# Performance work log

Measured on AMD Instinct MI355X. Metric: run time of the kernel, lower is better.

Reference implementation:

```python
import jax, jax.numpy as jnp
import numpy as np

ANNEAL = 0.01

def _tsig(x, temp=ANNEAL):
    # temperature sigmoid with +/-50 clipping as in the torch source
    return jax.nn.sigmoid(jnp.clip(x / temp, -50.0, 50.0))

def setup_inputs() -> dict:
    key = jax.random.key(0)
    k1, k2 = jax.random.split(key)
    N, D = 512, 512
    preds = jax.random.normal(k1, (N, D), dtype=jnp.float32)
    labels = jax.random.randint(k2, (N,), 0, 64, dtype=jnp.int64)
    return {"preds": preds, "labels": labels}

def reference(preds, labels):
    N = preds.shape[0]
    dtype = preds.dtype
    eye = jnp.eye(N, dtype=dtype)
    same = (labels[:, None] == labels[None, :]).astype(dtype)
    I_pos = same * (1.0 - eye)                      # positives excl. self
    sim_mat = preds @ preds.T                       # [N, N]
    # sim_diff[i, j, k] = sim_mat[i, k] - sim_mat[i, j]
    sim_sg = _tsig(sim_mat[:, None, :] - sim_mat[:, :, None]) * (1.0 - eye)[None, :, :]
    sim_all_rk = 1.0 + jnp.sum(sim_sg, axis=-1)     # [N, N]
    # sum_k sim_sg[i,j,k] * I_pos[i,k]
    pos_sum = jnp.einsum('ijk,ik->ij', sim_sg, I_pos)
    sim_pos_rk = eye + I_pos + I_pos * pos_sum      # [N, N]
    n_pos = jnp.sum(I_pos, axis=1) + 1.0            # [N]
    per_anchor = jnp.sum(sim_pos_rk / sim_all_rk, axis=1) / n_pos
    per_anchor = jnp.where(n_pos > 1.0, per_anchor, 0.0)  # skip anchors with no positives
    ap = jnp.sum(per_anchor) / N
    return 1.0 - ap
```

## Files before the change

kernel.cpp:

```cpp
#include <hip/hip_runtime.h>

#define NN 512
#define NB 256
#define FMAGIC 0x5AD0F1A6u

__global__ __launch_bounds__(512) void sap_fused(const float* __restrict__ P,
                                                 const int* __restrict__ labels,
                                                 unsigned* __restrict__ pa_bits,
                                                 unsigned* __restrict__ flags,
                                                 float* __restrict__ out) {
    __shared__ float arow[2][NN];
    __shared__ float srow[2][NN];
    __shared__ int   labels_sh[NN];
    __shared__ float posf2[2][NN];
    __shared__ int   poslist2[2][NN];
    __shared__ int   npos2[2];
    __shared__ float wave_part2[2][4];
    __shared__ float pa_out[2];
    __shared__ float sh[256];

    const int t    = threadIdx.x;
    const int lane = t & 63;
    const int wave = t >> 6;
    const int g    = lane & 15;
    const int grp  = lane >> 4;
    const int b    = blockIdx.x;
    const int i0   = b * 2;

    if (t < 128) ((int4*)labels_sh)[t] = ((const int4*)labels)[t];
    if (t < 256) ((float4*)&arow[0][0])[t] = ((const float4*)&P[i0 * NN])[t];
    __syncthreads();

    {
        const float4* A0 = (const float4*)&arow[0][0];
        const float4* A1 = (const float4*)&arow[1][0];
#pragma unroll 2
        for (int bb_ = 0; bb_ < 16; ++bb_) {
            const int k = wave * 64 + bb_ * 4 + grp;
            const float4* B = (const float4*)&P[k * NN];
            float s0 = 0.f, s1 = 0.f;
#pragma unroll
            for (int c = 0; c < 8; ++c) {
                const float4 bb = B[g + 16 * c];
                const float4 a0 = A0[g + 16 * c];
                const float4 a1 = A1[g + 16 * c];
                s0 += a0.x * bb.x; s0 += a0.y * bb.y;
                s0 += a0.z * bb.z; s0 += a0.w * bb.w;
                s1 += a1.x * bb.x; s1 += a1.y * bb.y;
                s1 += a1.z * bb.z; s1 += a1.w * bb.w;
            }
#pragma unroll
            for (int off = 1; off < 16; off <<= 1) {
                s0 += __shfl_xor(s0, off);
                s1 += __shfl_xor(s1, off);
            }
            if (g == 0) { srow[0][k] = s0; srow[1][k] = s1; }
        }
    }

    const float C1   = 100.0f * 1.44269504088896340736f;
    const float CLIP = 50.0f  * 1.44269504088896340736f;
    const int a  = wave >> 2;
    const int w4 = wave & 3;

    __syncthreads();
    if (t == 0) { npos2[0] = 0; npos2[1] = 0; }
    if (t < 8) wave_part2[t >> 2][t & 3] = 0.f;
    __syncthreads();
#pragma unroll
    for (int aa = 0; aa < 2; ++aa) {
        const int i  = i0 + aa;
        const int li = labels_sh[i];
        bool p = (labels_sh[t] == li) && (t != i);
        posf2[aa][t] = p ? 1.f : 0.f;
        if (p) { int idx = atomicAdd(&npos2[aa], 1); poslist2[aa][idx] = t; }
    }
    __syncthreads();

    {
        const int   i   = i0 + a;
        const int   cnt = npos2[a];
        float acc = 0.f;
        if (cnt > 0) {
            const float* sr = srow[a];
            const float* pf = posf2[a];
            const int*   pl = poslist2[a];
            for (int idx = w4; idx <= cnt; idx += 4) {
                const int   j   = (idx == cnt) ? i : pl[idx];
                const float sij = sr[j];
                float sum_all = 0.f, sum_pos = 0.f;
#pragma unroll
                for (int kk = 0; kk < 8; kk++) {
                    const int k = lane + (kk << 6);
                    float y = (sij - sr[k]) * C1;
                    y = fminf(fmaxf(y, -CLIP), CLIP);
                    float tt = 1.0f / (1.0f + exp2f(y));
                    if (k == j) tt = 0.f;
                    sum_all += tt;
                    sum_pos += tt * pf[k];
                }
#pragma unroll
                for (int off = 32; off; off >>= 1) {
                    sum_all += __shfl_down(sum_all, off);
                    sum_pos += __shfl_down(sum_pos, off);
                }
                if (lane == 0) {
                    const float den = 1.0f + sum_all;
                    acc += ((j == i) ? 1.0f : (1.0f + sum_pos)) / den;
                }
            }
        }
        if (lane == 0) wave_part2[a][w4] = acc;
    }
    __syncthreads();
    if (t == 0) {
#pragma unroll
        for (int aa = 0; aa < 2; ++aa) {
            const int cnt2 = npos2[aa];
            if (cnt2 == 0) { pa_out[aa] = 0.f; continue; }
            float tot = wave_part2[aa][0] + wave_part2[aa][1]
                      + wave_part2[aa][2] + wave_part2[aa][3];
            pa_out[aa] = tot / (float)(cnt2 + 1);
        }
    }
    __syncthreads();

    if (t == 0) {
        __hip_atomic_store(&pa_bits[i0],     __float_as_uint(pa_out[0]),
                           __ATOMIC_RELAXED, __HIP_MEMORY_SCOPE_AGENT);
        __hip_atomic_store(&pa_bits[i0 + 1], __float_as_uint(pa_out[1]),
                           __ATOMIC_RELAXED, __HIP_MEMORY_SCOPE_AGENT);
        asm volatile("s_waitcnt vmcnt(0)" ::: "memory");
        __hip_atomic_store(&flags[b], FMAGIC,
                           __ATOMIC_RELAXED, __HIP_MEMORY_SCOPE_AGENT);
    }

    if (b != 0) return;

    if (t < NB) {
        while (__hip_atomic_load(&flags[t], __ATOMIC_RELAXED,
                                 __HIP_MEMORY_SCOPE_AGENT) != FMAGIC)
            __builtin_amdgcn_s_sleep(8);
        __hip_atomic_store(&flags[t], 0u, __ATOMIC_RELAXED,
                           __HIP_MEMORY_SCOPE_AGENT);
    }
    __syncthreads();

    if (t < 256) {
        float v0 = __uint_as_float(__hip_atomic_load(&pa_bits[t], __ATOMIC_RELAXED,
                                                     __HIP_MEMORY_SCOPE_AGENT));
        float v1 = __uint_as_float(__hip_atomic_load(&pa_bits[t + 256], __ATOMIC_RELAXED,
                                                     __HIP_MEMORY_SCOPE_AGENT));
        sh[t] = v0 + v1;
    }
    __syncthreads();
    for (int s = 128; s; s >>= 1) {
        if (t < s) sh[t] += sh[t + s];
        __syncthreads();
    }
    if (t == 0) out[0] = 1.0f - sh[0] / (float)NN;
}

extern "C" void kernel_launch(void* const* d_in, const int* in_sizes, int n_in,
                              void* d_out, int out_size, void* d_ws, size_t ws_size,
                              hipStream_t stream) {
    const float* preds  = (const float*)d_in[0];
    const int*   labels = (const int*)d_in[1];
    float* out = (float*)d_out;

    unsigned* pa_bits = (unsigned*)d_ws;
    unsigned* flags   = pa_bits + NN;

    sap_fused<<<NB, 512, 0, stream>>>(preds, labels, pa_bits, flags, out);
}
```

Before: 73.80 us.

## Pair blocks to compute 4-row by half-column Gram tiles and exchange halves

```diff
diff --git a/kernel.cpp b/kernel.cpp
--- a/kernel.cpp
+++ b/kernel.cpp
@@ -2,14 +2,17 @@
 
 #define NN 512
 #define NB 256
+#define XMAGIC 0x7E31C9A5u
 #define FMAGIC 0x5AD0F1A6u
 
-__global__ __launch_bounds__(512) void sap_fused(const float* __restrict__ P,
-                                                 const int* __restrict__ labels,
-                                                 unsigned* __restrict__ pa_bits,
-                                                 unsigned* __restrict__ flags,
-                                                 float* __restrict__ out) {
-    __shared__ float arow[2][NN];
+__global__ __launch_bounds__(512, 2) void sap_fused(const float* __restrict__ P,
+                                                    const int* __restrict__ labels,
+                                                    unsigned* __restrict__ xch,
+                                                    unsigned* __restrict__ xflags,
+                                                    unsigned* __restrict__ pa_bits,
+                                                    unsigned* __restrict__ pflags,
+                                                    float* __restrict__ out) {
+    __shared__ float part[4][256];
     __shared__ float srow[2][NN];
     __shared__ int   labels_sh[NN];
     __shared__ float posf2[2][NN];
@@ -25,36 +28,93 @@
     const int g    = lane & 15;
     const int grp  = lane >> 4;
     const int b    = blockIdx.x;
+    const int p    = b ^ 1;
+    const int q    = b >> 1;
     const int i0   = b * 2;
+    const int half = b & 1;
+    const int H0   = half * 256;
 
     if (t < 128) ((int4*)labels_sh)[t] = ((const int4*)labels)[t];
-    if (t < 256) ((float4*)&arow[0][0])[t] = ((const float4*)&P[i0 * NN])[t];
-    __syncthreads();
-
-    {
-        const float4* A0 = (const float4*)&arow[0][0];
-        const float4* A1 = (const float4*)&arow[1][0];
+
+    float4 a0[8], a1[8], a2[8], a3[8];
+    {
+        const float4* A0 = (const float4*)&P[(4 * q + 0) * NN];
+        const float4* A1 = (const float4*)&P[(4 * q + 1) * NN];
+        const float4* A2 = (const float4*)&P[(4 * q + 2) * NN];
+        const float4* A3 = (const float4*)&P[(4 * q + 3) * NN];
+#pragma unroll
+        for (int c = 0; c < 8; ++c) {
+            a0[c] = A0[g + 16 * c];
+            a1[c] = A1[g + 16 * c];
+            a2[c] = A2[g + 16 * c];
+            a3[c] = A3[g + 16 * c];
+        }
+    }
+
 #pragma unroll 2
-        for (int bb_ = 0; bb_ < 16; ++bb_) {
-            const int k = wave * 64 + bb_ * 4 + grp;
-            const float4* B = (const float4*)&P[k * NN];
-            float s0 = 0.f, s1 = 0.f;
-#pragma unroll
-            for (int c = 0; c < 8; ++c) {
-                const float4 bb = B[g + 16 * c];
-                const float4 a0 = A0[g + 16 * c];
-                const float4 a1 = A1[g + 16 * c];
-                s0 += a0.x * bb.x; s0 += a0.y * bb.y;
-                s0 += a0.z * bb.z; s0 += a0.w * bb.w;
-                s1 += a1.x * bb.x; s1 += a1.y * bb.y;
-                s1 += a1.z * bb.z; s1 += a1.w * bb.w;
+    for (int bb_ = 0; bb_ < 8; ++bb_) {
+        const int k = H0 + wave * 32 + bb_ * 4 + grp;
+        const float4* B = (const float4*)&P[k * NN];
+        float s0 = 0.f, s1 = 0.f, s2 = 0.f, s3 = 0.f;
+#pragma unroll
+        for (int c = 0; c < 8; ++c) {
+            const float4 bb = B[g + 16 * c];
+            s0 += a0[c].x * bb.x; s0 += a0[c].y * bb.y;
+            s0 += a0[c].z * bb.z; s0 += a0[c].w * bb.w;
+            s1 += a1[c].x * bb.x; s1 += a1[c].y * bb.y;
+            s1 += a1[c].z * bb.z; s1 += a1[c].w * bb.w;
+            s2 += a2[c].x * bb.x; s2 += a2[c].y * bb.y;
+            s2 += a2[c].z * bb.z; s2 += a2[c].w * bb.w;
+            s3 += a3[c].x * bb.x; s3 += a3[c].y * bb.y;
+            s3 += a3[c].z * bb.z; s3 += a3[c].w * bb.w;
+        }
+#pragma unroll
+        for (int off = 1; off < 16; off <<= 1) {
+            s0 += __shfl_xor(s0, off);
+            s1 += __shfl_xor(s1, off);
+            s2 += __shfl_xor(s2, off);
+            s3 += __shfl_xor(s3, off);
+        }
+        if (g == 0) {
+            const int kk = k - H0;
+            part[0][kk] = s0; part[1][kk] = s1;
+            part[2][kk] = s2; part[3][kk] = s3;
+        }
+    }
+    __syncthreads();
+
+    {
+        const int up0 = 2 * (1 - half);
+        const int m   = t >> 8;
+        const int kk  = t & 255;
+        __hip_atomic_store(&xch[(size_t)b * 512 + m * 256 + kk],
+                           __float_as_uint(part[up0 + m][kk]),
+                           __ATOMIC_RELAXED, __HIP_MEMORY_SCOPE_AGENT);
+        asm volatile("s_waitcnt vmcnt(0)" ::: "memory");
+        __syncthreads();
+        if (t == 0)
+            __hip_atomic_store(&xflags[b], XMAGIC,
+                               __ATOMIC_RELAXED, __HIP_MEMORY_SCOPE_AGENT);
+    }
+
+    if (t == 0) {
+        while (__hip_atomic_load(&xflags[p], __ATOMIC_RELAXED,
+                                 __HIP_MEMORY_SCOPE_AGENT) != XMAGIC)
+            __builtin_amdgcn_s_sleep(2);
+    }
+    __syncthreads();
+    {
+        const int um0 = 2 * half;
+        const int Hp0 = (1 - half) * 256;
+#pragma unroll
+        for (int m = 0; m < 2; ++m) {
+            if (t >= H0 && t < H0 + 256) {
+                srow[m][t] = part[um0 + m][t - H0];
+            } else {
+                srow[m][t] = __uint_as_float(
+                    __hip_atomic_load(&xch[(size_t)p * 512 + m * 256 + (t - Hp0)],
+                                      __ATOMIC_RELAXED, __HIP_MEMORY_SCOPE_AGENT));
             }
-#pragma unroll
-            for (int off = 1; off < 16; off <<= 1) {
-                s0 += __shfl_xor(s0, off);
-                s1 += __shfl_xor(s1, off);
-            }
-            if (g == 0) { srow[0][k] = s0; srow[1][k] = s1; }
         }
     }
 
@@ -71,9 +131,9 @@
     for (int aa = 0; aa < 2; ++aa) {
         const int i  = i0 + aa;
         const int li = labels_sh[i];
-        bool p = (labels_sh[t] == li) && (t != i);
-        posf2[aa][t] = p ? 1.f : 0.f;
-        if (p) { int idx = atomicAdd(&npos2[aa], 1); poslist2[aa][idx] = t; }
+        bool pp = (labels_sh[t] == li) && (t != i);
+        posf2[aa][t] = pp ? 1.f : 0.f;
+        if (pp) { int idx = atomicAdd(&npos2[aa], 1); poslist2[aa][idx] = t; }
     }
     __syncthreads();
 
@@ -131,17 +191,19 @@
         __hip_atomic_store(&pa_bits[i0 + 1], __float_as_uint(pa_out[1]),
                            __ATOMIC_RELAXED, __HIP_MEMORY_SCOPE_AGENT);
         asm volatile("s_waitcnt vmcnt(0)" ::: "memory");
-        __hip_atomic_store(&flags[b], FMAGIC,
+        __hip_atomic_store(&pflags[b], FMAGIC,
                            __ATOMIC_RELAXED, __HIP_MEMORY_SCOPE_AGENT);
     }
 
     if (b != 0) return;
 
     if (t < NB) {
-        while (__hip_atomic_load(&flags[t], __ATOMIC_RELAXED,
+        while (__hip_atomic_load(&pflags[t], __ATOMIC_RELAXED,
                                  __HIP_MEMORY_SCOPE_AGENT) != FMAGIC)
             __builtin_amdgcn_s_sleep(8);
-        __hip_atomic_store(&flags[t], 0u, __ATOMIC_RELAXED,
+        __hip_atomic_store(&pflags[t], 0u, __ATOMIC_RELAXED,
+                           __HIP_MEMORY_SCOPE_AGENT);
+        __hip_atomic_store(&xflags[t], 0u, __ATOMIC_RELAXED,
                            __HIP_MEMORY_SCOPE_AGENT);
     }
     __syncthreads();
@@ -168,8 +230,11 @@
     const int*   labels = (const int*)d_in[1];
     float* out = (float*)d_out;
 
-    unsigned* pa_bits = (unsigned*)d_ws;
-    unsigned* flags   = pa_bits + NN;
-
-    sap_fused<<<NB, 512, 0, stream>>>(preds, labels, pa_bits, flags, out);
+    unsigned* xch     = (unsigned*)d_ws;
+    unsigned* xflags  = xch + NB * 512;
+    unsigned* pa_bits = xflags + NB;
+    unsigned* pflags  = pa_bits + NN;
+
+    sap_fused<<<NB, 512, 0, stream>>>(preds, labels, xch, xflags,
+                                      pa_bits, pflags, out);
 }
```

Result: slower. 82.46 us (+11.7%).
